# Performance work log

Measured on AMD Instinct MI355X. Metric: run time of the kernel, lower is better.

Reference implementation:

```python
import jax, jax.numpy as jnp
import numpy as np

F = 512        # filters (output channels)
C = 512        # input channels
H, W = 256, 256
DENSITY = 26214 / (F * C)  # ~0.1 nonzero fraction (sparsity ~0.9)


def setup_inputs() -> dict:
    key = jax.random.key(0)
    k1, k2, k3, k4 = jax.random.split(key, 4)
    inputs = jax.random.normal(k1, (1, C, H, W), dtype=jnp.float32)
    kernel_vals = jax.random.normal(k2, (F, C), dtype=jnp.float32)
    mask = jax.random.uniform(k3, (F, C)) < DENSITY  # uniform-sparsity connector
    kernel = jnp.where(mask, kernel_vals, 0.0)       # sparse kernel stored dense
    bias = jax.random.normal(k4, (F,), dtype=jnp.float32)
    return {"inputs": inputs, "kernel": kernel, "mask": mask, "bias": bias}


def reference(inputs, kernel, mask, bias):
    # 1x1 conv as spmm: flatten spatial dims -> [C, H*W], sparse kernel [F, C].
    _, c, h, w = inputs.shape
    flat_inputs = inputs.reshape(c, h * w)
    kernel_sp = jnp.where(mask, kernel, 0.0)
    # fused_spmm path: spmm + bias + relu
    flat_output = jax.nn.relu(kernel_sp @ flat_inputs + bias[:, None])
    return flat_output.reshape(1, -1, h, w)
```

## Files before the change

kernel.cpp:

```cpp
#include <hip/hip_runtime.h>
#include <stdint.h>


#define NF 512
#define NC 512
#define HW 65536
#define ELL_CAP 96
#define ELL_STRIDE 104
#define STRIP 64
#define ROWB 144

typedef __fp16 half2_t __attribute__((ext_vector_type(2)));

__global__ __launch_bounds__(256) void prep_ell(const float* __restrict__ kernel,
                                                int2* __restrict__ ell,
                                                int* __restrict__ cnt) {
  const int row = (blockIdx.x * 256 + threadIdx.x) >> 6;
  const int lane = threadIdx.x & 63;
  if (row >= NF) return;
  const float* krow = kernel + (size_t)row * NC;
  int2* erow = ell + (size_t)row * ELL_STRIDE;
  int n = 0;
  for (int step = 0; step < NC / 64; ++step) {
    const int c = step * 64 + lane;
    const float w = krow[c];
    const bool nz = (w != 0.0f);
    const unsigned long long m = __ballot(nz);
    const int pos = n + __popcll(m & ((1ull << lane) - 1ull));
    if (nz && pos < ELL_CAP) erow[pos] = make_int2(c * ROWB, __float_as_int(w));
    n += __popcll(m);
  }
  const int nn = n < ELL_CAP ? n : ELL_CAP;
  for (int p = nn + lane; p < ELL_STRIDE; p += 64) erow[p] = make_int2(0, 0);
  if (lane == 0) cnt[row] = nn;
}

__global__ __launch_bounds__(1024, 8) void spmm_main(
    const float* __restrict__ X, const int2* __restrict__ ell,
    const int* __restrict__ cnt, const float* __restrict__ bias,
    float* __restrict__ out) {
  __shared__ __align__(16) char ldsb[NC * ROWB];

  const int tid = threadIdx.x;
  const int wave = tid >> 6;
  const int lane = tid & 63;
  const int hw0 = blockIdx.x * STRIP;

  {
    const int rsub = lane >> 4;
    const int col = (lane & 15) * 4;
    for (int i = 0; i < 8; ++i) {
      const int r = wave * 32 + i * 4 + rsub;
      const float4 x4 = *(const float4*)(X + (size_t)r * HW + hw0 + col);
      const half2_t p0 = __builtin_amdgcn_cvt_pkrtz(x4.x, x4.y);
      const half2_t p1 = __builtin_amdgcn_cvt_pkrtz(x4.z, x4.w);
      uint2 p;
      p.x = __builtin_bit_cast(uint32_t, p0);
      p.y = __builtin_bit_cast(uint32_t, p1);
      *(uint2*)(ldsb + r * ROWB + col * 2) = p;
    }
  }
  __syncthreads();

  const int l8 = lane & 7;
  const int g = lane >> 3;
  const int lbase = l8 * 16;

  for (int fi = 0; fi < 4; ++fi) {
    const int f = wave * 32 + g * 4 + fi;
    int n = cnt[f];
    n = max(n, __shfl_xor(n, 8));
    n = max(n, __shfl_xor(n, 16));
    n = max(n, __shfl_xor(n, 32));
    const int quads = (n + 3) >> 2;
    const int4* e4 = (const int4*)(ell + (size_t)f * ELL_STRIDE);
    int4 pA = e4[0], pB = e4[1];
    float a0 = 0.f, a1 = 0.f, a2 = 0.f, a3 = 0.f;
    float a4 = 0.f, a5 = 0.f, a6 = 0.f, a7 = 0.f;

#define PROC(OFF, WB)                                                    \
    {                                                                    \
      const uint4 u = *(const uint4*)(ldsb + (OFF) + lbase);             \
      const float w = __int_as_float(WB);                                \
      const half2_t h0 = __builtin_bit_cast(half2_t, u.x);               \
      const half2_t h1 = __builtin_bit_cast(half2_t, u.y);               \
      const half2_t h2 = __builtin_bit_cast(half2_t, u.z);               \
      const half2_t h3 = __builtin_bit_cast(half2_t, u.w);               \
      a0 = fmaf(w, (float)h0.x, a0); a1 = fmaf(w, (float)h0.y, a1);      \
      a2 = fmaf(w, (float)h1.x, a2); a3 = fmaf(w, (float)h1.y, a3);      \
      a4 = fmaf(w, (float)h2.x, a4); a5 = fmaf(w, (float)h2.y, a5);      \
      a6 = fmaf(w, (float)h3.x, a6); a7 = fmaf(w, (float)h3.y, a7);      \
    }

    for (int q = 0; q < quads; ++q) {
      const int4 cA = pA, cB = pB;
      pA = e4[q * 2 + 2];
      pB = e4[q * 2 + 3];
      PROC(cA.x, cA.y);
      PROC(cA.z, cA.w);
      PROC(cB.x, cB.y);
      PROC(cB.z, cB.w);
    }
#undef PROC

    const float b = bias[f];
    float4 o0, o1;
    o0.x = fmaxf(a0 + b, 0.f); o0.y = fmaxf(a1 + b, 0.f);
    o0.z = fmaxf(a2 + b, 0.f); o0.w = fmaxf(a3 + b, 0.f);
    o1.x = fmaxf(a4 + b, 0.f); o1.y = fmaxf(a5 + b, 0.f);
    o1.z = fmaxf(a6 + b, 0.f); o1.w = fmaxf(a7 + b, 0.f);
    float* op = out + (size_t)f * HW + hw0 + l8 * 8;
    *(float4*)op = o0;
    *(float4*)(op + 4) = o1;
  }
}

extern "C" void kernel_launch(void* const* d_in, const int* in_sizes, int n_in,
                              void* d_out, int out_size, void* d_ws, size_t ws_size,
                              hipStream_t stream) {
  const float* X = (const float*)d_in[0];
  const float* kern = (const float*)d_in[1];
  const float* bias = (const float*)d_in[3];
  float* out = (float*)d_out;

  int2* ell = (int2*)d_ws;
  int* cnt = (int*)((char*)d_ws + (size_t)NF * ELL_STRIDE * sizeof(int2));

  prep_ell<<<NF * 64 / 256, 256, 0, stream>>>(kern, ell, cnt);
  spmm_main<<<HW / STRIP, 1024, 0, stream>>>(X, ell, cnt, bias, out);
}
```

Measured before the change: 329.6 us.

## Sort filter rows by nonzero count to balance per-wave sparse work

```diff
diff --git a/kernel.cpp b/kernel.cpp
--- a/kernel.cpp
+++ b/kernel.cpp
@@ -8,7 +8,7 @@
 #define ELL_CAP 96
 #define ELL_STRIDE 104
 #define STRIP 64
-#define ROWB 144
+#define ROWB 128
 
 typedef __fp16 half2_t __attribute__((ext_vector_type(2)));
 
@@ -35,10 +35,31 @@
   if (lane == 0) cnt[row] = nn;
 }
 
+__global__ __launch_bounds__(512) void prep_sort(const int* __restrict__ cnt,
+                                                 int* __restrict__ perm,
+                                                 int* __restrict__ chunkn) {
+  __shared__ int base[ELL_CAP + 1];
+  const int tid = threadIdx.x;
+  if (tid <= ELL_CAP) base[tid] = 0;
+  __syncthreads();
+  const int c = cnt[tid];
+  atomicAdd(&base[c], 1);
+  __syncthreads();
+  if (tid == 0) {
+    int run = 0;
+    for (int k = ELL_CAP; k >= 0; --k) { const int h = base[k]; base[k] = run; run += h; }
+  }
+  __syncthreads();
+  const int rank = atomicAdd(&base[c], 1);
+  perm[rank] = tid;
+  __syncthreads();
+  if (tid < NF / 8) chunkn[tid] = cnt[perm[tid * 8]];
+}
+
 __global__ __launch_bounds__(1024, 8) void spmm_main(
     const float* __restrict__ X, const int2* __restrict__ ell,
-    const int* __restrict__ cnt, const float* __restrict__ bias,
-    float* __restrict__ out) {
+    const int* __restrict__ perm, const int* __restrict__ chunkn,
+    const float* __restrict__ bias, float* __restrict__ out) {
   __shared__ __align__(16) char ldsb[NC * ROWB];
 
   const int tid = threadIdx.x;
@@ -48,16 +69,16 @@
 
   {
     const int rsub = lane >> 4;
-    const int col = (lane & 15) * 4;
+    const int colf = (lane & 15) * 4;
     for (int i = 0; i < 8; ++i) {
       const int r = wave * 32 + i * 4 + rsub;
-      const float4 x4 = *(const float4*)(X + (size_t)r * HW + hw0 + col);
+      const float4 x4 = *(const float4*)(X + (size_t)r * HW + hw0 + colf);
       const half2_t p0 = __builtin_amdgcn_cvt_pkrtz(x4.x, x4.y);
       const half2_t p1 = __builtin_amdgcn_cvt_pkrtz(x4.z, x4.w);
       uint2 p;
       p.x = __builtin_bit_cast(uint32_t, p0);
       p.y = __builtin_bit_cast(uint32_t, p1);
-      *(uint2*)(ldsb + r * ROWB + col * 2) = p;
+      *(uint2*)(ldsb + r * ROWB + colf * 2) = p;
     }
   }
   __syncthreads();
@@ -67,11 +88,9 @@
   const int lbase = l8 * 16;
 
   for (int fi = 0; fi < 4; ++fi) {
-    const int f = wave * 32 + g * 4 + fi;
-    int n = cnt[f];
-    n = max(n, __shfl_xor(n, 8));
-    n = max(n, __shfl_xor(n, 16));
-    n = max(n, __shfl_xor(n, 32));
+    const int chunk = fi * 16 + wave;
+    const int f = perm[chunk * 8 + g];
+    const int n = chunkn[chunk];
     const int quads = (n + 3) >> 2;
     const int4* e4 = (const int4*)(ell + (size_t)f * ELL_STRIDE);
     int4 pA = e4[0], pB = e4[1];
@@ -123,9 +142,13 @@
   const float* bias = (const float*)d_in[3];
   float* out = (float*)d_out;
 
-  int2* ell = (int2*)d_ws;
-  int* cnt = (int*)((char*)d_ws + (size_t)NF * ELL_STRIDE * sizeof(int2));
+  char* ws = (char*)d_ws;
+  int2* ell = (int2*)ws;
+  int* cnt = (int*)(ws + (size_t)NF * ELL_STRIDE * 8);
+  int* perm = cnt + NF;
+  int* chunkn = perm + NF;
 
   prep_ell<<<NF * 64 / 256, 256, 0, stream>>>(kern, ell, cnt);
-  spmm_main<<<HW / STRIP, 1024, 0, stream>>>(X, ell, cnt, bias, out);
+  prep_sort<<<1, 512, 0, stream>>>(cnt, perm, chunkn);
+  spmm_main<<<HW / STRIP, 1024, 0, stream>>>(X, ell, perm, chunkn, bias, out);
 }
```

Measured after the change: 318.9 us. 1.03x faster.
